# Optimization experiments

Hardware: AMD Instinct MI355X
Metric: run time of the kernel (lower is better)

## Reference

```python
import jax, jax.numpy as jnp
import numpy as np

HIDDEN = 1024
INTER = 256
N_EXPERTS = 16
B, T = 4, 2048
NEG_INF = -1000000000.0


def setup_inputs() -> dict:
    key = jax.random.key(0)
    ks = jax.random.split(key, 5)
    hidden_states = jax.random.normal(ks[0], (B, T, HIDDEN), dtype=jnp.float32)
    sim_matrix = jax.random.normal(ks[1], (HIDDEN, N_EXPERTS), dtype=jnp.float32)
    threshold = jnp.zeros((1,), dtype=jnp.float32)
    # torch Linear weights: w1 [I, C], w2 [C, I]; store per-expert stacked in
    # matmul-friendly layout: w1 [E, C, I], w2 [E, I, C]
    w1 = jax.random.normal(ks[2], (N_EXPERTS, HIDDEN, INTER), dtype=jnp.float32) / np.sqrt(HIDDEN)
    w2 = jax.random.normal(ks[3], (N_EXPERTS, INTER, HIDDEN), dtype=jnp.float32) / np.sqrt(INTER)
    return {"hidden_states": hidden_states, "sim_matrix": sim_matrix,
            "threshold": threshold, "w1": w1, "w2": w2}


def _l2norm(x, axis):
    return x / jnp.maximum(jnp.linalg.norm(x, axis=axis, keepdims=True), 1e-12)


def reference(hidden_states, sim_matrix, threshold, w1, w2):
    Bq, Tq, C = hidden_states.shape
    x = hidden_states.reshape(-1, C)                      # [N, C]
    # gate
    scores = _l2norm(x, -1) @ _l2norm(sim_matrix, 0)      # [N, E]
    activated = scores > threshold
    k_per_token = activated.sum(axis=-1)                  # [N] int
    masked = jnp.where(activated, scores, NEG_INF)
    routing_weights = jax.nn.softmax(masked, axis=-1)     # [N, E]
    # dense all-expert FFN
    h = jax.nn.gelu(jnp.einsum('nc,eci->nei', x, w1), approximate=False)
    out = jnp.einsum('nei,eic->nec', h, w2)               # [N, E, C]
    final = jnp.einsum('nec,ne->nc', out, routing_weights)
    return final.reshape(Bq, Tq, C), scores, k_per_token
```

## Files before the change

### kernel.cpp

```cpp
#include <hip/hip_runtime.h>
#include <hip/hip_bf16.h>
#include <math.h>

#define NTOK 8192
#define HID  1024
#define ISZ  256
#define NEXP 16
#define NBIG 4096

typedef __attribute__((ext_vector_type(8))) short bf16x8;
typedef __attribute__((ext_vector_type(4))) float f32x4;

#define MFMA16(a, b, c) __builtin_amdgcn_mfma_f32_16x16x32_bf16(a, b, c, 0, 0, 0)

__device__ __forceinline__ unsigned short f2bf(float f) {
  unsigned u = __float_as_uint(f);
  u += 0x7fff + ((u >> 16) & 1);
  return (unsigned short)(u >> 16);
}

__device__ __forceinline__ void async16(void* l, const void* g) {
  __builtin_amdgcn_global_load_lds(
      (const __attribute__((address_space(1))) unsigned int*)g,
      (__attribute__((address_space(3))) unsigned int*)l, 16, 0, 0);
}

__global__ void simnorm_kernel(const float* __restrict__ sm, float* __restrict__ inv_smn) {
  __shared__ float red[16][17];
  int t = threadIdx.x;
  int e = t & 15, g = t >> 4;
  float ss = 0.f;
  for (int c = g; c < HID; c += 16) {
    float v = sm[c * NEXP + e];
    ss += v * v;
  }
  red[e][g] = ss;
  __syncthreads();
  if (t < 16) {
    float s = 0.f;
    #pragma unroll
    for (int i = 0; i < 16; i++) s += red[t][i];
    inv_smn[t] = 1.f / fmaxf(sqrtf(s), 1e-12f);
  }
}

__global__ __launch_bounds__(256)
void gate_kernel(const float* __restrict__ x, const float* __restrict__ sm,
                 const float* __restrict__ thr, const float* __restrict__ inv_smn,
                 float* __restrict__ scores_out, float* __restrict__ k_out,
                 float* __restrict__ rw_out, unsigned short* __restrict__ xb_out) {
  const int n = blockIdx.x;
  const int t = threadIdx.x;
  const int lane = t & 63, wave = t >> 6;
  const float* xr = x + (size_t)n * HID;

  float p[16];
  #pragma unroll
  for (int e = 0; e < 16; e++) p[e] = 0.f;
  float ss = 0.f;

  #pragma unroll
  for (int q = 0; q < 4; q++) {
    int c = t + q * 256;
    float v = xr[c];
    ss += v * v;
    xb_out[(size_t)n * HID + c] = f2bf(v);
    const float4* smr = (const float4*)(sm + (size_t)c * NEXP);
    float4 s0 = smr[0], s1 = smr[1], s2 = smr[2], s3 = smr[3];
    p[0] += v * s0.x;  p[1] += v * s0.y;  p[2] += v * s0.z;  p[3] += v * s0.w;
    p[4] += v * s1.x;  p[5] += v * s1.y;  p[6] += v * s1.z;  p[7] += v * s1.w;
    p[8] += v * s2.x;  p[9] += v * s2.y;  p[10] += v * s2.z; p[11] += v * s2.w;
    p[12] += v * s3.x; p[13] += v * s3.y; p[14] += v * s3.z; p[15] += v * s3.w;
  }

  #pragma unroll
  for (int off = 32; off > 0; off >>= 1) {
    ss += __shfl_down(ss, off, 64);
    #pragma unroll
    for (int e = 0; e < 16; e++) p[e] += __shfl_down(p[e], off, 64);
  }

  __shared__ float red[4][17];
  __shared__ float sc[16];
  if (lane == 0) {
    red[wave][0] = ss;
    #pragma unroll
    for (int e = 0; e < 16; e++) red[wave][1 + e] = p[e];
  }
  __syncthreads();

  if (t < 16) {
    float d = red[0][1 + t] + red[1][1 + t] + red[2][1 + t] + red[3][1 + t];
    float ssum = red[0][0] + red[1][0] + red[2][0] + red[3][0];
    float inv_x = 1.f / fmaxf(sqrtf(ssum), 1e-12f);
    float s = d * inv_x * inv_smn[t];
    scores_out[(size_t)n * 16 + t] = s;
    sc[t] = s;
  }
  __syncthreads();

  if (t < 16) {
    float thrv = thr[0];
    float s = sc[t];
    bool act = s > thrv;
    float m = act ? s : -INFINITY;
    int cnt = act ? 1 : 0;
    #pragma unroll
    for (int off = 8; off > 0; off >>= 1) {
      m = fmaxf(m, __shfl_xor(m, off, 16));
      cnt += __shfl_xor(cnt, off, 16);
    }
    float pv;
    if (cnt > 0) pv = act ? expf(s - m) : 0.f;
    else         pv = 1.f;
    float sum = pv;
    #pragma unroll
    for (int off = 8; off > 0; off >>= 1) sum += __shfl_xor(sum, off, 16);
    rw_out[(size_t)n * 16 + t] = pv / sum;
    if (t == 0) k_out[n] = (float)cnt;
  }
}

__global__ __launch_bounds__(256)
void transpose_cast_kernel(const float* __restrict__ src, unsigned short* __restrict__ dst,
                           int R, int C, int dstride, int e_src_stride, int e_dst_mult) {
  __shared__ float tile[32][33];
  const int e = blockIdx.z;
  const int r0 = blockIdx.y * 32, c0 = blockIdx.x * 32;
  const int tx = threadIdx.x & 31, ty = threadIdx.x >> 5;
  const float* s = src + (size_t)e * e_src_stride;
  #pragma unroll
  for (int q = 0; q < 4; q++) {
    int r = r0 + ty + q * 8;
    tile[ty + q * 8][tx] = s[(size_t)r * C + c0 + tx];
  }
  __syncthreads();
  unsigned short* d = dst + (size_t)e * e_dst_mult;
  #pragma unroll
  for (int q = 0; q < 4; q++) {
    int cc = c0 + ty + q * 8;
    int r  = r0 + tx;
    d[(size_t)cc * dstride + r] = f2bf(tile[tx][ty + q * 8]);
  }
}

template <int KEXT, int LD, int NBN>
__global__ __launch_bounds__(512, 2)
void gemm1_k(const unsigned short* __restrict__ A, const unsigned short* __restrict__ B,
             unsigned short* __restrict__ Cb, const float* __restrict__ rw) {
  __shared__ __align__(1024) char lds[65536];
  constexpr int NT = KEXT / 64;
  const int tid = threadIdx.x;
  const int lane = tid & 63, wid = tid >> 6;
  const int wm = wid >> 2, wn = wid & 3;
  const int lr = lane & 15;

  const int nwg = gridDim.x, cpx = nwg >> 3;
  const int wg = (blockIdx.x & 7) * cpx + (blockIdx.x >> 3);
  const int bm = wg / NBN, bn = wg % NBN;

  const int swz = (lr & 7) << 4;
  const int colk0 = ((lane >> 4) * 16) ^ swz;
  const int colk1 = (64 + (lane >> 4) * 16) ^ swz;
  const int wmo = wm * 16384, wno = wn * 8192, lro = lr * 128;

  int sRow[4], sCol[4], so[4];
  #pragma unroll
  for (int i = 0; i < 4; i++) {
    int o = (i * 512 + tid) * 16;
    so[i] = o;
    int r = o >> 7, cb = o & 127;
    sRow[i] = r; sCol[i] = (cb ^ ((r & 7) << 4)) >> 1;
  }

  const unsigned short* Ag = A + (size_t)bm * 256 * LD;
  const unsigned short* Bg = B + (size_t)bn * 256 * LD;

  f32x4 acc[8][4];
  #pragma unroll
  for (int m = 0; m < 8; m++)
    #pragma unroll
    for (int n = 0; n < 4; n++) acc[m][n] = (f32x4){0.f, 0.f, 0.f, 0.f};

  #pragma unroll 1
  for (int t = 0; t < NT; ++t) {
    const int kt = t * 64;
    #pragma unroll
    for (int i = 0; i < 4; i++) {
      async16(lds + so[i],         Ag + (size_t)sRow[i] * LD + kt + sCol[i]);
      async16(lds + 32768 + so[i], Bg + (size_t)sRow[i] * LD + kt + sCol[i]);
    }
    __syncthreads();

    {
      bf16x8 a[8], b[4];
      #pragma unroll
      for (int mf = 0; mf < 8; mf++)
        a[mf] = *(const bf16x8*)(lds + wmo + mf * 2048 + lro + colk0);
      #pragma unroll
      for (int nf = 0; nf < 4; nf++)
        b[nf] = *(const bf16x8*)(lds + 32768 + wno + nf * 2048 + lro + colk0);
      #pragma unroll
      for (int mf = 0; mf < 8; mf++)
        #pragma unroll
        for (int nf = 0; nf < 4; nf++)
          acc[mf][nf] = MFMA16(a[mf], b[nf], acc[mf][nf]);
    }
    {
      bf16x8 a[8], b[4];
      #pragma unroll
      for (int mf = 0; mf < 8; mf++)
        a[mf] = *(const bf16x8*)(lds + wmo + mf * 2048 + lro + colk1);
      #pragma unroll
      for (int nf = 0; nf < 4; nf++)
        b[nf] = *(const bf16x8*)(lds + 32768 + wno + nf * 2048 + lro + colk1);
      #pragma unroll
      for (int mf = 0; mf < 8; mf++)
        #pragma unroll
        for (int nf = 0; nf < 4; nf++)
          acc[mf][nf] = MFMA16(a[mf], b[nf], acc[mf][nf]);
    }
    __syncthreads();
  }

  const int jr = (lane >> 4) * 4;
  float wrow[8][4];
  #pragma unroll
  for (int m = 0; m < 8; m++)
    #pragma unroll
    for (int j = 0; j < 4; j++)
      wrow[m][j] = rw[(size_t)(bm * 256 + wm * 128 + m * 16 + jr + j) * 16 + bn];
  #pragma unroll
  for (int m = 0; m < 8; m++) {
    #pragma unroll
    for (int n = 0; n < 4; n++) {
      int col = bn * 256 + wn * 64 + n * 16 + lr;
      #pragma unroll
      for (int j = 0; j < 4; j++) {
        int r = bm * 256 + wm * 128 + m * 16 + jr + j;
        float v = acc[m][n][j];
        float g = 0.7978845608f * (v + 0.044715f * v * v * v);
        float e = __expf(2.f * g);
        float th = 1.f - 2.f / (e + 1.f);
        float ge = 0.5f * v * (1.f + th);
        Cb[(size_t)r * NBIG + col] = f2bf(ge * wrow[m][j]);
      }
    }
  }
}

#define G2PHASE(CK, STG, WAIT_)                                                \
  {                                                                            \
    bf16x8 afr[4], bfr[4];                                                     \
    _Pragma("unroll")                                                          \
    for (int ml = 0; ml < 4; ml++)                                             \
      afr[ml] = *(const bf16x8*)(bufA + wmo + ml*2048 + lro + (CK));           \
    _Pragma("unroll")                                                          \
    for (int nl = 0; nl < 4; nl++)                                             \
      bfr[nl] = *(const bf16x8*)(bufB + wno + nl*2048 + lro + (CK));           \
    if (STG) {                                                                 \
      _Pragma("unroll")                                                        \
      for (int i = 0; i < 2; i++)                                              \
        async16(ldsAn + o16[i], Ag + (size_t)aRow[i]*K + kn + aCol[i]);        \
      _Pragma("unroll")                                                        \
      for (int i = 0; i < 4; i++)                                              \
        async16(ldsBn + o16b[i], Bg + (size_t)bRow[i]*K + kn + bCol[i]);       \
    }                                                                          \
    __builtin_amdgcn_sched_barrier(0);                                         \
    __builtin_amdgcn_s_barrier();                                              \
    asm volatile("s_waitcnt lgkmcnt(0)" ::: "memory");                         \
    __builtin_amdgcn_sched_barrier(0);                                         \
    __builtin_amdgcn_s_setprio(1);                                             \
    _Pragma("unroll")                                                          \
    for (int m4 = 0; m4 < 4; m4++)                                             \
      _Pragma("unroll")                                                        \
      for (int n4 = 0; n4 < 4; n4++)                                           \
        acc[m4][n4] = MFMA16(afr[m4], bfr[n4], acc[m4][n4]);                   \
    __builtin_amdgcn_s_setprio(0);                                             \
    __builtin_amdgcn_sched_barrier(0);                                         \
    if (WAIT_) { asm volatile("s_waitcnt vmcnt(0)" ::: "memory"); }            \
    __builtin_amdgcn_s_barrier();                                              \
    __builtin_amdgcn_sched_barrier(0);                                         \
  }

template <int K>
__global__ __launch_bounds__(512, 2)
void gemm2_k(const unsigned short* __restrict__ A, const unsigned short* __restrict__ B,
             float* __restrict__ Cf) {
  __shared__ __align__(1024) char lds[98304];
  constexpr int NT = K / 64;
  const int tid = threadIdx.x;
  const int lane = tid & 63, wid = tid >> 6;
  const int wm = wid >> 2, wn = wid & 3;
  const int lr = lane & 15;

  const int wg = (blockIdx.x & 7) * 32 + (blockIdx.x >> 3);
  const int bm = wg >> 2, bn = wg & 3;

  const int swz = (lr & 7) << 4;
  const int colk0 = ((lane >> 4) * 16) ^ swz;
  const int colk1 = (64 + (lane >> 4) * 16) ^ swz;
  const int wmo = wm * 8192, wno = wn * 8192, lro = lr * 128;

  int aRow[2], aCol[2], o16[2];
  int bRow[4], bCol[4], o16b[4];
  #pragma unroll
  for (int i = 0; i < 2; i++) {
    int o = (i * 512 + tid) * 16;
    o16[i] = o;
    int r = o >> 7, cb = o & 127;
    aRow[i] = r; aCol[i] = (cb ^ ((r & 7) << 4)) >> 1;
  }
  #pragma unroll
  for (int i = 0; i < 4; i++) {
    int o = (i * 512 + tid) * 16;
    o16b[i] = o;
    int r = o >> 7, cb = o & 127;
    bRow[i] = r; bCol[i] = (cb ^ ((r & 7) << 4)) >> 1;
  }

  const unsigned short* Ag = A + (size_t)bm * 128 * K;
  const unsigned short* Bg = B + (size_t)bn * 256 * K;

  f32x4 acc[4][4];
  #pragma unroll
  for (int m = 0; m < 4; m++)
    #pragma unroll
    for (int n = 0; n < 4; n++) acc[m][n] = (f32x4){0.f, 0.f, 0.f, 0.f};

  #pragma unroll
  for (int i = 0; i < 2; i++) async16(lds + o16[i],          Ag + (size_t)aRow[i] * K + aCol[i]);
  #pragma unroll
  for (int i = 0; i < 4; i++) async16(lds + 32768 + o16b[i], Bg + (size_t)bRow[i] * K + bCol[i]);
  asm volatile("s_waitcnt vmcnt(0)" ::: "memory");
  __builtin_amdgcn_s_barrier();

  #pragma unroll 1
  for (int t = 0; t < NT; t += 2) {
    {
      const char* bufA = lds;
      const char* bufB = lds + 32768;
      char* ldsAn = lds + 16384;
      char* ldsBn = lds + 32768 + 32768;
      const int kn = ((t + 1) & (NT - 1)) << 6;
      G2PHASE(colk0, 1, 0)
      G2PHASE(colk1, 0, 1)
    }
    {
      const char* bufA = lds + 16384;
      const char* bufB = lds + 32768 + 32768;
      char* ldsAn = lds;
      char* ldsBn = lds + 32768;
      const int kn = ((t + 2) & (NT - 1)) << 6;
      G2PHASE(colk0, 1, 0)
      G2PHASE(colk1, 0, 1)
    }
  }

  asm volatile("s_waitcnt vmcnt(0)" ::: "memory");

  const int jr = (lane >> 4) * 4;
  #pragma unroll
  for (int m = 0; m < 4; m++) {
    #pragma unroll
    for (int n = 0; n < 4; n++) {
      int col = bn * 256 + wn * 64 + n * 16 + lr;
      #pragma unroll
      for (int j = 0; j < 4; j++) {
        int r = bm * 128 + wm * 64 + m * 16 + jr + j;
        Cf[(size_t)r * HID + col] = acc[m][n][j];
      }
    }
  }
}

extern "C" void kernel_launch(void* const* d_in, const int* in_sizes, int n_in,
                              void* d_out, int out_size, void* d_ws, size_t ws_size,
                              hipStream_t stream) {
  const float* x   = (const float*)d_in[0];
  const float* sm  = (const float*)d_in[1];
  const float* thr = (const float*)d_in[2];
  const float* w1  = (const float*)d_in[3];
  const float* w2  = (const float*)d_in[4];

  float* out_final  = (float*)d_out;
  float* out_scores = out_final + (size_t)NTOK * HID;
  float* out_k      = out_scores + (size_t)NTOK * NEXP;

  char* ws = (char*)d_ws;
  size_t off = 0;
  float* inv_smn = (float*)(ws + off); off += 256;
  float* rwbuf   = (float*)(ws + off); off += (size_t)NTOK * NEXP * 4;
  unsigned short* Xb  = (unsigned short*)(ws + off); off += (size_t)NTOK * HID * 2;
  unsigned short* W1T = (unsigned short*)(ws + off); off += (size_t)NBIG * HID * 2;
  unsigned short* W2T = (unsigned short*)(ws + off); off += (size_t)HID * NBIG * 2;
  unsigned short* H   = (unsigned short*)(ws + off); off += (size_t)NTOK * NBIG * 2;

  simnorm_kernel<<<1, 256, 0, stream>>>(sm, inv_smn);
  gate_kernel<<<NTOK, 256, 0, stream>>>(x, sm, thr, inv_smn, out_scores, out_k, rwbuf, Xb);
  transpose_cast_kernel<<<dim3(ISZ / 32, HID / 32, NEXP), 256, 0, stream>>>(
      w1, W1T, HID, ISZ, HID, HID * ISZ, ISZ * HID);
  transpose_cast_kernel<<<dim3(HID / 32, ISZ / 32, NEXP), 256, 0, stream>>>(
      w2, W2T, ISZ, HID, NBIG, ISZ * HID, ISZ);

  gemm1_k<HID, HID, 16><<<512, 512, 0, stream>>>(Xb, W1T, H, rwbuf);
  gemm2_k<NBIG><<<256, 512, 0, stream>>>(H, W2T, out_final);
}
```

Measured before the change: 229.7 us.

## Pre-pack GEMM1 operands into MFMA fragment layout and load directly to registers

Adds repack kernels that rearrange the bf16 activations and W1 into an MFMA-fragment-major layout, so each lane's 16-byte operand is contiguous in global memory. GEMM1 then drops its LDS staging and barriers and loads fragments straight from global into registers, with a two-stage register double buffer. This removes LDS traffic and syncthreads. In exchange it adds an extra pass over the activations, and it loses the LDS reuse across waves, so each wave now reads A and B from global/L2 on its own.

Result: slower. 270.8 us (+17.9%).

```diff
diff --git a/kernel.cpp b/kernel.cpp
--- a/kernel.cpp
+++ b/kernel.cpp
@@ -144,12 +144,60 @@
   }
 }
 
-template <int KEXT, int LD, int NBN>
+__global__ __launch_bounds__(256)
+void transpose_cast_frag(const float* __restrict__ w1, unsigned short* __restrict__ W1F) {
+  __shared__ float tile[32][33];
+  const int e = blockIdx.z;
+  const int r0 = blockIdx.y * 32, c0 = blockIdx.x * 32;
+  const int tx = threadIdx.x & 31, ty = threadIdx.x >> 5;
+  const float* s = w1 + (size_t)e * (HID * ISZ);
+  #pragma unroll
+  for (int q = 0; q < 4; q++) {
+    int r = r0 + ty + q * 8;
+    tile[ty + q * 8][tx] = s[(size_t)r * ISZ + c0 + tx];
+  }
+  __syncthreads();
+  const int t = threadIdx.x;
+  if (t < 128) {
+    const int sc = t & 31, gg = t >> 5;
+    const int gi = e * ISZ + c0 + sc;
+    const int k  = r0 + gg * 8;
+    const int rowblk = gi >> 4, lr = gi & 15;
+    bf16x8 v;
+    #pragma unroll
+    for (int j = 0; j < 8; j++) v[j] = (short)f2bf(tile[gg * 8 + j][sc]);
+    size_t base = ((size_t)rowblk * 2048 + (size_t)(k >> 5) * 64 + ((k >> 3) & 3) * 16 + lr) * 8;
+    *(bf16x8*)(W1F + base) = v;
+  }
+}
+
+__global__ __launch_bounds__(256)
+void repack_frag(const unsigned short* __restrict__ Xb, unsigned short* __restrict__ XbF) {
+  __shared__ unsigned short lds2[16 * 1032];
+  const int b = blockIdx.x;
+  const int t = threadIdx.x;
+  #pragma unroll
+  for (int j = 0; j < 8; j++) {
+    int s = t + 256 * j;
+    int row = s >> 7, kseg = s & 127;
+    bf16x8 v = *(const bf16x8*)(Xb + ((size_t)(b * 16 + row)) * HID + kseg * 8);
+    *(bf16x8*)(&lds2[row * 1032 + kseg * 8]) = v;
+  }
+  __syncthreads();
+  #pragma unroll
+  for (int j = 0; j < 8; j++) {
+    int s2 = t + 256 * j;
+    int l = s2 & 63, kb = s2 >> 6;
+    int row = l & 15, k = kb * 32 + (l >> 4) * 8;
+    bf16x8 v = *(const bf16x8*)(&lds2[row * 1032 + k]);
+    *(bf16x8*)(XbF + (size_t)b * 16384 + (size_t)s2 * 8) = v;
+  }
+}
+
+template <int KO, int NBN>
 __global__ __launch_bounds__(512, 2)
-void gemm1_k(const unsigned short* __restrict__ A, const unsigned short* __restrict__ B,
-             unsigned short* __restrict__ Cb, const float* __restrict__ rw) {
-  __shared__ __align__(1024) char lds[65536];
-  constexpr int NT = KEXT / 64;
+void gemm1_frag(const unsigned short* __restrict__ XbF, const unsigned short* __restrict__ W1F,
+                unsigned short* __restrict__ Cb, const float* __restrict__ rw) {
   const int tid = threadIdx.x;
   const int lane = tid & 63, wid = tid >> 6;
   const int wm = wid >> 2, wn = wid & 3;
@@ -159,22 +207,8 @@
   const int wg = (blockIdx.x & 7) * cpx + (blockIdx.x >> 3);
   const int bm = wg / NBN, bn = wg % NBN;
 
-  const int swz = (lr & 7) << 4;
-  const int colk0 = ((lane >> 4) * 16) ^ swz;
-  const int colk1 = (64 + (lane >> 4) * 16) ^ swz;
-  const int wmo = wm * 16384, wno = wn * 8192, lro = lr * 128;
-
-  int sRow[4], sCol[4], so[4];
-  #pragma unroll
-  for (int i = 0; i < 4; i++) {
-    int o = (i * 512 + tid) * 16;
-    so[i] = o;
-    int r = o >> 7, cb = o & 127;
-    sRow[i] = r; sCol[i] = (cb ^ ((r & 7) << 4)) >> 1;
-  }
-
-  const unsigned short* Ag = A + (size_t)bm * 256 * LD;
-  const unsigned short* Bg = B + (size_t)bn * 256 * LD;
+  const unsigned short* Ab = XbF + ((size_t)(bm * 16 + wm * 8) * 2048 + lane) * 8;
+  const unsigned short* Bb = W1F + ((size_t)(bn * 16 + wn * 4) * 2048 + lane) * 8;
 
   f32x4 acc[8][4];
   #pragma unroll
@@ -182,45 +216,34 @@
     #pragma unroll
     for (int n = 0; n < 4; n++) acc[m][n] = (f32x4){0.f, 0.f, 0.f, 0.f};
 
+  bf16x8 a0[8], b0[4], a1[8], b1[4];
+  #pragma unroll
+  for (int mf = 0; mf < 8; mf++) a0[mf] = *(const bf16x8*)(Ab + mf * 16384);
+  #pragma unroll
+  for (int nf = 0; nf < 4; nf++) b0[nf] = *(const bf16x8*)(Bb + nf * 16384);
+
   #pragma unroll 1
-  for (int t = 0; t < NT; ++t) {
-    const int kt = t * 64;
-    #pragma unroll
-    for (int i = 0; i < 4; i++) {
-      async16(lds + so[i],         Ag + (size_t)sRow[i] * LD + kt + sCol[i]);
-      async16(lds + 32768 + so[i], Bg + (size_t)sRow[i] * LD + kt + sCol[i]);
-    }
-    __syncthreads();
-
-    {
-      bf16x8 a[8], b[4];
-      #pragma unroll
-      for (int mf = 0; mf < 8; mf++)
-        a[mf] = *(const bf16x8*)(lds + wmo + mf * 2048 + lro + colk0);
+  for (int ko = 0; ko < KO; ko += 2) {
+    const int k1 = ko + 1;
+    const int k2 = (ko + 2) & (KO - 1);
+    #pragma unroll
+    for (int mf = 0; mf < 8; mf++) a1[mf] = *(const bf16x8*)(Ab + mf * 16384 + k1 * 512);
+    #pragma unroll
+    for (int nf = 0; nf < 4; nf++) b1[nf] = *(const bf16x8*)(Bb + nf * 16384 + k1 * 512);
+    #pragma unroll
+    for (int mf = 0; mf < 8; mf++)
       #pragma unroll
       for (int nf = 0; nf < 4; nf++)
-        b[nf] = *(const bf16x8*)(lds + 32768 + wno + nf * 2048 + lro + colk0);
-      #pragma unroll
-      for (int mf = 0; mf < 8; mf++)
-        #pragma unroll
-        for (int nf = 0; nf < 4; nf++)
-          acc[mf][nf] = MFMA16(a[mf], b[nf], acc[mf][nf]);
-    }
-    {
-      bf16x8 a[8], b[4];
-      #pragma unroll
-      for (int mf = 0; mf < 8; mf++)
-        a[mf] = *(const bf16x8*)(lds + wmo + mf * 2048 + lro + colk1);
+        acc[mf][nf] = MFMA16(a0[mf], b0[nf], acc[mf][nf]);
+    #pragma unroll
+    for (int mf = 0; mf < 8; mf++) a0[mf] = *(const bf16x8*)(Ab + mf * 16384 + k2 * 512);
+    #pragma unroll
+    for (int nf = 0; nf < 4; nf++) b0[nf] = *(const bf16x8*)(Bb + nf * 16384 + k2 * 512);
+    #pragma unroll
+    for (int mf = 0; mf < 8; mf++)
       #pragma unroll
       for (int nf = 0; nf < 4; nf++)
-        b[nf] = *(const bf16x8*)(lds + 32768 + wno + nf * 2048 + lro + colk1);
-      #pragma unroll
-      for (int mf = 0; mf < 8; mf++)
-        #pragma unroll
-        for (int nf = 0; nf < 4; nf++)
-          acc[mf][nf] = MFMA16(a[mf], b[nf], acc[mf][nf]);
-    }
-    __syncthreads();
+        acc[mf][nf] = MFMA16(a1[mf], b1[nf], acc[mf][nf]);
   }
 
   const int jr = (lane >> 4) * 4;
@@ -392,17 +415,18 @@
   float* inv_smn = (float*)(ws + off); off += 256;
   float* rwbuf   = (float*)(ws + off); off += (size_t)NTOK * NEXP * 4;
   unsigned short* Xb  = (unsigned short*)(ws + off); off += (size_t)NTOK * HID * 2;
-  unsigned short* W1T = (unsigned short*)(ws + off); off += (size_t)NBIG * HID * 2;
+  unsigned short* XbF = (unsigned short*)(ws + off); off += (size_t)NTOK * HID * 2;
+  unsigned short* W1F = (unsigned short*)(ws + off); off += (size_t)NBIG * HID * 2;
   unsigned short* W2T = (unsigned short*)(ws + off); off += (size_t)HID * NBIG * 2;
   unsigned short* H   = (unsigned short*)(ws + off); off += (size_t)NTOK * NBIG * 2;
 
   simnorm_kernel<<<1, 256, 0, stream>>>(sm, inv_smn);
   gate_kernel<<<NTOK, 256, 0, stream>>>(x, sm, thr, inv_smn, out_scores, out_k, rwbuf, Xb);
-  transpose_cast_kernel<<<dim3(ISZ / 32, HID / 32, NEXP), 256, 0, stream>>>(
-      w1, W1T, HID, ISZ, HID, HID * ISZ, ISZ * HID);
+  repack_frag<<<512, 256, 0, stream>>>(Xb, XbF);
+  transpose_cast_frag<<<dim3(ISZ / 32, HID / 32, NEXP), 256, 0, stream>>>(w1, W1F);
   transpose_cast_kernel<<<dim3(HID / 32, ISZ / 32, NEXP), 256, 0, stream>>>(
       w2, W2T, ISZ, HID, NBIG, ISZ * HID, ISZ);
 
-  gemm1_k<HID, HID, 16><<<512, 512, 0, stream>>>(Xb, W1T, H, rwbuf);
+  gemm1_frag<HID / 32, 16><<<512, 512, 0, stream>>>(XbF, W1F, H, rwbuf);
   gemm2_k<NBIG><<<256, 512, 0, stream>>>(H, W2T, out_final);
 }
```

## Double-buffer gemm1 with split-phase async loads and triple-buffer gemm2

Applied to the files above, without the earlier changes.

gemm1 moves from a single-buffered load-sync-compute loop to a double-buffered pipeline. Each 64-wide K tile is split into four MFMA quadrants, and the next tile's A/B halves are issued asynchronously between them, with partial vmcnt waits and setprio around the MFMA bursts. gemm2 goes from double to triple buffering, prefetching two tiles ahead with vmcnt(6) waits instead of draining every load. The goal is to hide global-to-LDS latency behind MFMA work. In exchange, gemm1's LDS grows to 128KB, which likely drops it to one workgroup per CU, and gemm2's LDS grows to 144KB.

After: 226.8 us. About the same (-1.3%).

```diff
diff --git a/kernel.cpp b/kernel.cpp
--- a/kernel.cpp
+++ b/kernel.cpp
@@ -144,11 +144,102 @@
   }
 }
 
+#define FENCE_PRE()                                        \
+    __builtin_amdgcn_sched_barrier(0);                     \
+    __builtin_amdgcn_s_barrier();                          \
+    asm volatile("s_waitcnt lgkmcnt(0)" ::: "memory");     \
+    __builtin_amdgcn_sched_barrier(0);                     \
+    __builtin_amdgcn_s_setprio(1);
+
+#define FENCE_POST_W4()                                    \
+    __builtin_amdgcn_s_setprio(0);                         \
+    __builtin_amdgcn_sched_barrier(0);                     \
+    asm volatile("s_waitcnt vmcnt(4)" ::: "memory");       \
+    __builtin_amdgcn_s_barrier();                          \
+    __builtin_amdgcn_sched_barrier(0);
+
+#define FENCE_POST_W6()                                    \
+    __builtin_amdgcn_s_setprio(0);                         \
+    __builtin_amdgcn_sched_barrier(0);                     \
+    asm volatile("s_waitcnt vmcnt(6)" ::: "memory");       \
+    __builtin_amdgcn_s_barrier();                          \
+    __builtin_amdgcn_sched_barrier(0);
+
+#define FENCE_POST_NOW()                                   \
+    __builtin_amdgcn_s_setprio(0);                         \
+    __builtin_amdgcn_sched_barrier(0);                     \
+    __builtin_amdgcn_s_barrier();                          \
+    __builtin_amdgcn_sched_barrier(0);
+
+#define SU_A0(dst, kn) { async16((dst) + o16[0], Ag + (size_t)aRow[0] * LD + (kn) + aCol[0]); \
+                         async16((dst) + o16[1], Ag + (size_t)aRow[1] * LD + (kn) + aCol[1]); }
+#define SU_A1(dst, kn) { async16((dst) + 16384 + o16[0], Ag + (size_t)(aRow[0] + 64) * LD + (kn) + aCol[0]); \
+                         async16((dst) + 16384 + o16[1], Ag + (size_t)(aRow[1] + 64) * LD + (kn) + aCol[1]); }
+#define SU_B0(dst, kn) { async16((dst) + o16[0], Bg + (size_t)bRow[0] * LD + (kn) + bCol[0]); \
+                         async16((dst) + o16[1], Bg + (size_t)bRow[1] * LD + (kn) + bCol[1]); }
+#define SU_B1(dst, kn) { async16((dst) + 16384 + o16[0], Bg + (size_t)(bRow[0] + 32) * LD + (kn) + bCol[0]); \
+                         async16((dst) + 16384 + o16[1], Bg + (size_t)(bRow[1] + 32) * LD + (kn) + bCol[1]); }
+
+#define G1_TILE(bufA, bufB, ldsAn, ldsBn, kn)                                       \
+  {                                                                                 \
+    bf16x8 a0[4][2], a1[4][2], b0[2][2], b1[2][2];                                  \
+                                  \
+    _Pragma("unroll") for (int ml = 0; ml < 4; ml++) {                              \
+      a0[ml][0] = *(const bf16x8*)((bufA) + wmo + ml*2048 + lro + colk0);           \
+      a0[ml][1] = *(const bf16x8*)((bufA) + wmo + ml*2048 + lro + colk1);           \
+    }                                                                               \
+    _Pragma("unroll") for (int nl = 0; nl < 2; nl++) {                              \
+      b0[nl][0] = *(const bf16x8*)((bufB) + wno + nl*2048 + lro + colk0);           \
+      b0[nl][1] = *(const bf16x8*)((bufB) + wno + nl*2048 + lro + colk1);           \
+    }                                                                               \
+    SU_A0(ldsAn, kn) SU_B0(ldsBn, kn)                                               \
+    FENCE_PRE()                                                                     \
+    _Pragma("unroll") for (int ml = 0; ml < 4; ml++)                                \
+      _Pragma("unroll") for (int nl = 0; nl < 2; nl++) {                            \
+        acc[ml][nl] = MFMA16(a0[ml][0], b0[nl][0], acc[ml][nl]);                    \
+        acc[ml][nl] = MFMA16(a0[ml][1], b0[nl][1], acc[ml][nl]);                    \
+      }                                                                             \
+    FENCE_POST_W4()                                                                 \
+                                         \
+    _Pragma("unroll") for (int ml = 0; ml < 4; ml++) {                              \
+      a1[ml][0] = *(const bf16x8*)((bufA) + 16384 + wmo + ml*2048 + lro + colk0);   \
+      a1[ml][1] = *(const bf16x8*)((bufA) + 16384 + wmo + ml*2048 + lro + colk1);   \
+    }                                                                               \
+    SU_A1(ldsAn, kn) SU_B1(ldsBn, kn)                                               \
+    FENCE_PRE()                                                                     \
+    _Pragma("unroll") for (int ml = 0; ml < 4; ml++)                                \
+      _Pragma("unroll") for (int nl = 0; nl < 2; nl++) {                            \
+        acc[4 + ml][nl] = MFMA16(a1[ml][0], b0[nl][0], acc[4 + ml][nl]);            \
+        acc[4 + ml][nl] = MFMA16(a1[ml][1], b0[nl][1], acc[4 + ml][nl]);            \
+      }                                                                             \
+    FENCE_POST_NOW()                                                                \
+                                                        \
+    _Pragma("unroll") for (int nl = 0; nl < 2; nl++) {                              \
+      b1[nl][0] = *(const bf16x8*)((bufB) + 16384 + wno + nl*2048 + lro + colk0);   \
+      b1[nl][1] = *(const bf16x8*)((bufB) + 16384 + wno + nl*2048 + lro + colk1);   \
+    }                                                                               \
+    FENCE_PRE()                                                                     \
+    _Pragma("unroll") for (int ml = 0; ml < 4; ml++)                                \
+      _Pragma("unroll") for (int nl = 0; nl < 2; nl++) {                            \
+        acc[4 + ml][2 + nl] = MFMA16(a1[ml][0], b1[nl][0], acc[4 + ml][2 + nl]);    \
+        acc[4 + ml][2 + nl] = MFMA16(a1[ml][1], b1[nl][1], acc[4 + ml][2 + nl]);    \
+      }                                                                             \
+    FENCE_POST_NOW()                                                                \
+                                                          \
+    FENCE_PRE()                                                                     \
+    _Pragma("unroll") for (int ml = 0; ml < 4; ml++)                                \
+      _Pragma("unroll") for (int nl = 0; nl < 2; nl++) {                            \
+        acc[ml][2 + nl] = MFMA16(a0[ml][0], b1[nl][0], acc[ml][2 + nl]);            \
+        acc[ml][2 + nl] = MFMA16(a0[ml][1], b1[nl][1], acc[ml][2 + nl]);            \
+      }                                                                             \
+    FENCE_POST_W4()                                                                 \
+  }
+
 template <int KEXT, int LD, int NBN>
 __global__ __launch_bounds__(512, 2)
 void gemm1_k(const unsigned short* __restrict__ A, const unsigned short* __restrict__ B,
              unsigned short* __restrict__ Cb, const float* __restrict__ rw) {
-  __shared__ __align__(1024) char lds[65536];
+  __shared__ __align__(1024) char lds[131072];
   constexpr int NT = KEXT / 64;
   const int tid = threadIdx.x;
   const int lane = tid & 63, wid = tid >> 6;
@@ -162,15 +253,17 @@
   const int swz = (lr & 7) << 4;
   const int colk0 = ((lane >> 4) * 16) ^ swz;
   const int colk1 = (64 + (lane >> 4) * 16) ^ swz;
-  const int wmo = wm * 16384, wno = wn * 8192, lro = lr * 128;
-
-  int sRow[4], sCol[4], so[4];
-  #pragma unroll
-  for (int i = 0; i < 4; i++) {
+  const int wmo = wm * 8192, wno = wn * 4096, lro = lr * 128;
+
+  int aRow[2], aCol[2], bRow[2], bCol[2], o16[2];
+  #pragma unroll
+  for (int i = 0; i < 2; i++) {
     int o = (i * 512 + tid) * 16;
-    so[i] = o;
-    int r = o >> 7, cb = o & 127;
-    sRow[i] = r; sCol[i] = (cb ^ ((r & 7) << 4)) >> 1;
+    o16[i] = o;
+    { int wmb = o >> 13, ob = o & 8191, r = ob >> 7, cb = ob & 127;
+      aRow[i] = wmb * 128 + r; aCol[i] = (cb ^ ((r & 7) << 4)) >> 1; }
+    { int wnb = o >> 12, ob = o & 4095, r = ob >> 7, cb = ob & 127;
+      bRow[i] = wnb * 64 + r; bCol[i] = (cb ^ ((r & 7) << 4)) >> 1; }
   }
 
   const unsigned short* Ag = A + (size_t)bm * 256 * LD;
@@ -182,46 +275,24 @@
     #pragma unroll
     for (int n = 0; n < 4; n++) acc[m][n] = (f32x4){0.f, 0.f, 0.f, 0.f};
 
+  char* const b0A = lds;
+  char* const b1A = lds + 32768;
+  char* const b0B = lds + 65536;
+  char* const b1B = lds + 98304;
+
+  SU_A0(b0A, 0) SU_B0(b0B, 0)
+  SU_A1(b0A, 0) SU_B1(b0B, 0)
+  asm volatile("s_waitcnt vmcnt(4)" ::: "memory");
+  __builtin_amdgcn_s_barrier();
+  __builtin_amdgcn_sched_barrier(0);
+
   #pragma unroll 1
-  for (int t = 0; t < NT; ++t) {
-    const int kt = t * 64;
-    #pragma unroll
-    for (int i = 0; i < 4; i++) {
-      async16(lds + so[i],         Ag + (size_t)sRow[i] * LD + kt + sCol[i]);
-      async16(lds + 32768 + so[i], Bg + (size_t)sRow[i] * LD + kt + sCol[i]);
-    }
-    __syncthreads();
-
-    {
-      bf16x8 a[8], b[4];
-      #pragma unroll
-      for (int mf = 0; mf < 8; mf++)
-        a[mf] = *(const bf16x8*)(lds + wmo + mf * 2048 + lro + colk0);
-      #pragma unroll
-      for (int nf = 0; nf < 4; nf++)
-        b[nf] = *(const bf16x8*)(lds + 32768 + wno + nf * 2048 + lro + colk0);
-      #pragma unroll
-      for (int mf = 0; mf < 8; mf++)
-        #pragma unroll
-        for (int nf = 0; nf < 4; nf++)
-          acc[mf][nf] = MFMA16(a[mf], b[nf], acc[mf][nf]);
-    }
-    {
-      bf16x8 a[8], b[4];
-      #pragma unroll
-      for (int mf = 0; mf < 8; mf++)
-        a[mf] = *(const bf16x8*)(lds + wmo + mf * 2048 + lro + colk1);
-      #pragma unroll
-      for (int nf = 0; nf < 4; nf++)
-        b[nf] = *(const bf16x8*)(lds + 32768 + wno + nf * 2048 + lro + colk1);
-      #pragma unroll
-      for (int mf = 0; mf < 8; mf++)
-        #pragma unroll
-        for (int nf = 0; nf < 4; nf++)
-          acc[mf][nf] = MFMA16(a[mf], b[nf], acc[mf][nf]);
-    }
-    __syncthreads();
-  }
+  for (int t = 0; t < NT; t += 2) {
+    G1_TILE(b0A, b0B, b1A, b1B, (((t + 1) & (NT - 1)) << 6))
+    G1_TILE(b1A, b1B, b0A, b0B, (((t + 2) & (NT - 1)) << 6))
+  }
+
+  asm volatile("s_waitcnt vmcnt(0)" ::: "memory");
 
   const int jr = (lane >> 4) * 4;
   float wrow[8][4];
@@ -249,45 +320,11 @@
   }
 }
 
-#define G2PHASE(CK, STG, WAIT_)                                                \
-  {                                                                            \
-    bf16x8 afr[4], bfr[4];                                                     \
-    _Pragma("unroll")                                                          \
-    for (int ml = 0; ml < 4; ml++)                                             \
-      afr[ml] = *(const bf16x8*)(bufA + wmo + ml*2048 + lro + (CK));           \
-    _Pragma("unroll")                                                          \
-    for (int nl = 0; nl < 4; nl++)                                             \
-      bfr[nl] = *(const bf16x8*)(bufB + wno + nl*2048 + lro + (CK));           \
-    if (STG) {                                                                 \
-      _Pragma("unroll")                                                        \
-      for (int i = 0; i < 2; i++)                                              \
-        async16(ldsAn + o16[i], Ag + (size_t)aRow[i]*K + kn + aCol[i]);        \
-      _Pragma("unroll")                                                        \
-      for (int i = 0; i < 4; i++)                                              \
-        async16(ldsBn + o16b[i], Bg + (size_t)bRow[i]*K + kn + bCol[i]);       \
-    }                                                                          \
-    __builtin_amdgcn_sched_barrier(0);                                         \
-    __builtin_amdgcn_s_barrier();                                              \
-    asm volatile("s_waitcnt lgkmcnt(0)" ::: "memory");                         \
-    __builtin_amdgcn_sched_barrier(0);                                         \
-    __builtin_amdgcn_s_setprio(1);                                             \
-    _Pragma("unroll")                                                          \
-    for (int m4 = 0; m4 < 4; m4++)                                             \
-      _Pragma("unroll")                                                        \
-      for (int n4 = 0; n4 < 4; n4++)                                           \
-        acc[m4][n4] = MFMA16(afr[m4], bfr[n4], acc[m4][n4]);                   \
-    __builtin_amdgcn_s_setprio(0);                                             \
-    __builtin_amdgcn_sched_barrier(0);                                         \
-    if (WAIT_) { asm volatile("s_waitcnt vmcnt(0)" ::: "memory"); }            \
-    __builtin_amdgcn_s_barrier();                                              \
-    __builtin_amdgcn_sched_barrier(0);                                         \
-  }
-
 template <int K>
 __global__ __launch_bounds__(512, 2)
 void gemm2_k(const unsigned short* __restrict__ A, const unsigned short* __restrict__ B,
              float* __restrict__ Cf) {
-  __shared__ __align__(1024) char lds[98304];
+  __shared__ __align__(1024) char lds[147456];
   constexpr int NT = K / 64;
   const int tid = threadIdx.x;
   const int lane = tid & 63, wid = tid >> 6;
@@ -322,6 +359,9 @@
   const unsigned short* Ag = A + (size_t)bm * 128 * K;
   const unsigned short* Bg = B + (size_t)bn * 256 * K;
 
+  char* const ldsA = lds;
+  char* const ldsB = lds + 49152;
+
   f32x4 acc[4][4];
   #pragma unroll
   for (int m = 0; m < 4; m++)
@@ -329,32 +369,62 @@
     for (int n = 0; n < 4; n++) acc[m][n] = (f32x4){0.f, 0.f, 0.f, 0.f};
 
   #pragma unroll
-  for (int i = 0; i < 2; i++) async16(lds + o16[i],          Ag + (size_t)aRow[i] * K + aCol[i]);
-  #pragma unroll
-  for (int i = 0; i < 4; i++) async16(lds + 32768 + o16b[i], Bg + (size_t)bRow[i] * K + bCol[i]);
-  asm volatile("s_waitcnt vmcnt(0)" ::: "memory");
+  for (int s = 0; s < 2; s++) {
+    const int kk = s << 6;
+    #pragma unroll
+    for (int i = 0; i < 2; i++) async16(ldsA + s * 16384 + o16[i],  Ag + (size_t)aRow[i] * K + kk + aCol[i]);
+    #pragma unroll
+    for (int i = 0; i < 4; i++) async16(ldsB + s * 32768 + o16b[i], Bg + (size_t)bRow[i] * K + kk + bCol[i]);
+  }
+  asm volatile("s_waitcnt vmcnt(6)" ::: "memory");
   __builtin_amdgcn_s_barrier();
-
+  __builtin_amdgcn_sched_barrier(0);
+
+  int c0 = 0, c1 = 16384, c2 = 32768;
   #pragma unroll 1
-  for (int t = 0; t < NT; t += 2) {
+  for (int t = 0; t < NT; ++t) {
+    const char* bufA = ldsA + c0;
+    const char* bufB = ldsB + c0 * 2;
+    char* wA = ldsA + c2;
+    char* wB = ldsB + c2 * 2;
+    const int kn = ((t + 2) & (NT - 1)) << 6;
     {
-      const char* bufA = lds;
-      const char* bufB = lds + 32768;
-      char* ldsAn = lds + 16384;
-      char* ldsBn = lds + 32768 + 32768;
-      const int kn = ((t + 1) & (NT - 1)) << 6;
-      G2PHASE(colk0, 1, 0)
-      G2PHASE(colk1, 0, 1)
+      bf16x8 afr[4], bfr[4];
+      #pragma unroll
+      for (int ml = 0; ml < 4; ml++)
+        afr[ml] = *(const bf16x8*)(bufA + wmo + ml * 2048 + lro + colk0);
+      #pragma unroll
+      for (int nl = 0; nl < 4; nl++)
+        bfr[nl] = *(const bf16x8*)(bufB + wno + nl * 2048 + lro + colk0);
+      #pragma unroll
+      for (int i = 0; i < 2; i++) async16(wA + o16[i],  Ag + (size_t)aRow[i] * K + kn + aCol[i]);
+      #pragma unroll
+      for (int i = 0; i < 4; i++) async16(wB + o16b[i], Bg + (size_t)bRow[i] * K + kn + bCol[i]);
+      FENCE_PRE()
+      #pragma unroll
+      for (int m4 = 0; m4 < 4; m4++)
+        #pragma unroll
+        for (int n4 = 0; n4 < 4; n4++)
+          acc[m4][n4] = MFMA16(afr[m4], bfr[n4], acc[m4][n4]);
+      FENCE_POST_NOW()
     }
     {
-      const char* bufA = lds + 16384;
-      const char* bufB = lds + 32768 + 32768;
-      char* ldsAn = lds;
-      char* ldsBn = lds + 32768;
-      const int kn = ((t + 2) & (NT - 1)) << 6;
-      G2PHASE(colk0, 1, 0)
-      G2PHASE(colk1, 0, 1)
+      bf16x8 afr[4], bfr[4];
+      #pragma unroll
+      for (int ml = 0; ml < 4; ml++)
+        afr[ml] = *(const bf16x8*)(bufA + wmo + ml * 2048 + lro + colk1);
+      #pragma unroll
+      for (int nl = 0; nl < 4; nl++)
+        bfr[nl] = *(const bf16x8*)(bufB + wno + nl * 2048 + lro + colk1);
+      FENCE_PRE()
+      #pragma unroll
+      for (int m4 = 0; m4 < 4; m4++)
+        #pragma unroll
+        for (int n4 = 0; n4 < 4; n4++)
+          acc[m4][n4] = MFMA16(afr[m4], bfr[n4], acc[m4][n4]);
+      FENCE_POST_W6()
     }
+    int tmp = c0; c0 = c1; c1 = c2; c2 = tmp;
   }
 
   asm volatile("s_waitcnt vmcnt(0)" ::: "memory");
```

## Retile first expert GEMM to 128x128 blocks and vectorize gate loads

Applied to the files above, without the earlier changes.

The first GEMM moves from 256x256 tiles with 512 threads and K-step 64 to 128x128 tiles with 256 threads, K-step 32, 16KB of LDS and a new swizzle. This raises the block count to 2048 and targets more resident blocks per CU for better latency hiding and load balance. The cost is lower arithmetic intensity per block and more global traffic. Separately, the gate kernel now reads x as float4 and stores four bf16 values packed into one store, which changes which columns each thread handles.

New measurement: 252.1 us. 1.1x slower.

```diff
diff --git a/kernel.cpp b/kernel.cpp
--- a/kernel.cpp
+++ b/kernel.cpp
@@ -59,18 +59,26 @@
   for (int e = 0; e < 16; e++) p[e] = 0.f;
   float ss = 0.f;
 
-  #pragma unroll
-  for (int q = 0; q < 4; q++) {
-    int c = t + q * 256;
-    float v = xr[c];
+  float4 xv = ((const float4*)xr)[t];
+  float vs[4] = {xv.x, xv.y, xv.z, xv.w};
+  unsigned short xb4[4];
+  #pragma unroll
+  for (int j = 0; j < 4; j++) {
+    float v = vs[j];
     ss += v * v;
-    xb_out[(size_t)n * HID + c] = f2bf(v);
-    const float4* smr = (const float4*)(sm + (size_t)c * NEXP);
+    xb4[j] = f2bf(v);
+    const float4* smr = (const float4*)(sm + (size_t)(t * 4 + j) * NEXP);
     float4 s0 = smr[0], s1 = smr[1], s2 = smr[2], s3 = smr[3];
     p[0] += v * s0.x;  p[1] += v * s0.y;  p[2] += v * s0.z;  p[3] += v * s0.w;
     p[4] += v * s1.x;  p[5] += v * s1.y;  p[6] += v * s1.z;  p[7] += v * s1.w;
     p[8] += v * s2.x;  p[9] += v * s2.y;  p[10] += v * s2.z; p[11] += v * s2.w;
     p[12] += v * s3.x; p[13] += v * s3.y; p[14] += v * s3.z; p[15] += v * s3.w;
+  }
+  {
+    unsigned int lo = (unsigned)xb4[0] | ((unsigned)xb4[1] << 16);
+    unsigned int hi = (unsigned)xb4[2] | ((unsigned)xb4[3] << 16);
+    uint2 u; u.x = lo; u.y = hi;
+    ((uint2*)(xb_out + (size_t)n * HID))[t] = u;
   }
 
   #pragma unroll
@@ -145,103 +153,90 @@
 }
 
 template <int KEXT, int LD, int NBN>
-__global__ __launch_bounds__(512, 2)
-void gemm1_k(const unsigned short* __restrict__ A, const unsigned short* __restrict__ B,
-             unsigned short* __restrict__ Cb, const float* __restrict__ rw) {
-  __shared__ __align__(1024) char lds[65536];
-  constexpr int NT = KEXT / 64;
+__global__ __launch_bounds__(256, 3)
+void gemm1_m97(const unsigned short* __restrict__ A, const unsigned short* __restrict__ B,
+               unsigned short* __restrict__ Cb, const float* __restrict__ rw) {
+  __shared__ __align__(1024) char lds[16384];
+  constexpr int NT = KEXT / 32;
   const int tid = threadIdx.x;
   const int lane = tid & 63, wid = tid >> 6;
-  const int wm = wid >> 2, wn = wid & 3;
+  const int wm = wid >> 1, wn = wid & 1;
   const int lr = lane & 15;
 
   const int nwg = gridDim.x, cpx = nwg >> 3;
   const int wg = (blockIdx.x & 7) * cpx + (blockIdx.x >> 3);
   const int bm = wg / NBN, bn = wg % NBN;
 
-  const int swz = (lr & 7) << 4;
-  const int colk0 = ((lane >> 4) * 16) ^ swz;
-  const int colk1 = (64 + (lane >> 4) * 16) ^ swz;
-  const int wmo = wm * 16384, wno = wn * 8192, lro = lr * 128;
-
-  int sRow[4], sCol[4], so[4];
-  #pragma unroll
-  for (int i = 0; i < 4; i++) {
-    int o = (i * 512 + tid) * 16;
+  const int colr = ((lane >> 4) * 16) ^ (((lr >> 1) & 3) << 4);
+  int aoff[4], boff[4];
+  #pragma unroll
+  for (int f = 0; f < 4; f++) {
+    aoff[f] = (wm * 64 + f * 16 + lr) * 64 + colr;
+    boff[f] = 8192 + (wn * 64 + f * 16 + lr) * 64 + colr;
+  }
+
+  int sRow[2], sCol[2], so[2];
+  #pragma unroll
+  for (int i = 0; i < 2; i++) {
+    int o = (i * 256 + tid) * 16;
     so[i] = o;
-    int r = o >> 7, cb = o & 127;
-    sRow[i] = r; sCol[i] = (cb ^ ((r & 7) << 4)) >> 1;
-  }
-
-  const unsigned short* Ag = A + (size_t)bm * 256 * LD;
-  const unsigned short* Bg = B + (size_t)bn * 256 * LD;
-
-  f32x4 acc[8][4];
-  #pragma unroll
-  for (int m = 0; m < 8; m++)
+    int r = o >> 6, cb = o & 63;
+    sRow[i] = r; sCol[i] = (cb ^ (((r >> 1) & 3) << 4)) >> 1;
+  }
+
+  const unsigned short* Ag = A + (size_t)bm * 128 * LD;
+  const unsigned short* Bg = B + (size_t)bn * 128 * LD;
+
+  f32x4 acc[4][4];
+  #pragma unroll
+  for (int m = 0; m < 4; m++)
     #pragma unroll
     for (int n = 0; n < 4; n++) acc[m][n] = (f32x4){0.f, 0.f, 0.f, 0.f};
 
   #pragma unroll 1
   for (int t = 0; t < NT; ++t) {
-    const int kt = t * 64;
-    #pragma unroll
-    for (int i = 0; i < 4; i++) {
-      async16(lds + so[i],         Ag + (size_t)sRow[i] * LD + kt + sCol[i]);
-      async16(lds + 32768 + so[i], Bg + (size_t)sRow[i] * LD + kt + sCol[i]);
+    const int kt = t * 32;
+    #pragma unroll
+    for (int i = 0; i < 2; i++) {
+      async16(lds + so[i],        Ag + (size_t)sRow[i] * LD + kt + sCol[i]);
+      async16(lds + 8192 + so[i], Bg + (size_t)sRow[i] * LD + kt + sCol[i]);
     }
     __syncthreads();
 
-    {
-      bf16x8 a[8], b[4];
-      #pragma unroll
-      for (int mf = 0; mf < 8; mf++)
-        a[mf] = *(const bf16x8*)(lds + wmo + mf * 2048 + lro + colk0);
+    bf16x8 a[4], b[4];
+    #pragma unroll
+    for (int f = 0; f < 4; f++) a[f] = *(const bf16x8*)(lds + aoff[f]);
+    #pragma unroll
+    for (int f = 0; f < 4; f++) b[f] = *(const bf16x8*)(lds + boff[f]);
+    #pragma unroll
+    for (int mf = 0; mf < 4; mf++)
       #pragma unroll
       for (int nf = 0; nf < 4; nf++)
-        b[nf] = *(const bf16x8*)(lds + 32768 + wno + nf * 2048 + lro + colk0);
-      #pragma unroll
-      for (int mf = 0; mf < 8; mf++)
-        #pragma unroll
-        for (int nf = 0; nf < 4; nf++)
-          acc[mf][nf] = MFMA16(a[mf], b[nf], acc[mf][nf]);
-    }
-    {
-      bf16x8 a[8], b[4];
-      #pragma unroll
-      for (int mf = 0; mf < 8; mf++)
-        a[mf] = *(const bf16x8*)(lds + wmo + mf * 2048 + lro + colk1);
-      #pragma unroll
-      for (int nf = 0; nf < 4; nf++)
-        b[nf] = *(const bf16x8*)(lds + 32768 + wno + nf * 2048 + lro + colk1);
-      #pragma unroll
-      for (int mf = 0; mf < 8; mf++)
-        #pragma unroll
-        for (int nf = 0; nf < 4; nf++)
-          acc[mf][nf] = MFMA16(a[mf], b[nf], acc[mf][nf]);
-    }
+        acc[mf][nf] = MFMA16(a[mf], b[nf], acc[mf][nf]);
+
     __syncthreads();
   }
 
   const int jr = (lane >> 4) * 4;
-  float wrow[8][4];
-  #pragma unroll
-  for (int m = 0; m < 8; m++)
+  const int e = bn >> 1;
+  float wrow[4][4];
+  #pragma unroll
+  for (int m = 0; m < 4; m++)
     #pragma unroll
     for (int j = 0; j < 4; j++)
-      wrow[m][j] = rw[(size_t)(bm * 256 + wm * 128 + m * 16 + jr + j) * 16 + bn];
-  #pragma unroll
-  for (int m = 0; m < 8; m++) {
+      wrow[m][j] = rw[(size_t)(bm * 128 + wm * 64 + m * 16 + jr + j) * 16 + e];
+  #pragma unroll
+  for (int m = 0; m < 4; m++) {
     #pragma unroll
     for (int n = 0; n < 4; n++) {
-      int col = bn * 256 + wn * 64 + n * 16 + lr;
+      int col = bn * 128 + wn * 64 + n * 16 + lr;
       #pragma unroll
       for (int j = 0; j < 4; j++) {
-        int r = bm * 256 + wm * 128 + m * 16 + jr + j;
+        int r = bm * 128 + wm * 64 + m * 16 + jr + j;
         float v = acc[m][n][j];
         float g = 0.7978845608f * (v + 0.044715f * v * v * v);
-        float e = __expf(2.f * g);
-        float th = 1.f - 2.f / (e + 1.f);
+        float ex = __expf(2.f * g);
+        float th = 1.f - 2.f / (ex + 1.f);
         float ge = 0.5f * v * (1.f + th);
         Cb[(size_t)r * NBIG + col] = f2bf(ge * wrow[m][j]);
       }
@@ -403,6 +398,6 @@
   transpose_cast_kernel<<<dim3(HID / 32, ISZ / 32, NEXP), 256, 0, stream>>>(
       w2, W2T, ISZ, HID, NBIG, ISZ * HID, ISZ);
 
-  gemm1_k<HID, HID, 16><<<512, 512, 0, stream>>>(Xb, W1T, H, rwbuf);
+  gemm1_m97<HID, HID, 32><<<2048, 256, 0, stream>>>(Xb, W1T, H, rwbuf);
   gemm2_k<NBIG><<<256, 512, 0, stream>>>(H, W2T, out_final);
 }
```
